# Kernel tuning notes

Measured on AMD Instinct MI355X. Metric: run time of the kernel, lower is better.

## Reference

```python
import jax, jax.numpy as jnp
import numpy as np

TAU = 0.001
TEMPERATURE = 0.1


def setup_inputs() -> dict:
    key = jax.random.key(0)
    k1, k2 = jax.random.split(key)
    B, H, N, L = 2, 8, 256, 64
    X = jax.random.normal(k1, (B, H, N, L), dtype=jnp.float32)
    Y = jax.random.normal(k2, (B, H, N, L), dtype=jnp.float32)
    return {"X": X, "Y": Y}


def _softsort_p2(scores):
    # scores: [B,H,N,L] -> s: [B,H,L,N]
    s = jnp.transpose(scores, (0, 1, 3, 2))
    srt = -jnp.sort(-s, axis=-1)  # descending sort along N
    # pairwise squared diff: rows = sorted values, cols = original values -> [B,H,L,N,N]
    pd = -((s[..., None, :] - srt[..., :, None]) ** 2) / TAU
    return jax.nn.softmax(pd, axis=-1)


def reference(X, Y):
    # Soft permutation matrices: [B,H,L,N,N]
    Pu = _softsort_p2(X)
    Pv = _softsort_p2(Y)
    # Gamma = Pu^T @ Pv  (contract over sorted-row index i)
    Gamma = jnp.einsum('bhlij,bhlik->bhljk', Pu, Pv)
    # cdist(X, Y, p=2) over last dim L -> [B,H,N,N]
    x2 = jnp.sum(X * X, axis=-1)            # [B,H,N]
    y2 = jnp.sum(Y * Y, axis=-1)            # [B,H,N]
    xy = jnp.einsum('bhnl,bhml->bhnm', X, Y)
    cost = jnp.sqrt(jnp.maximum(x2[..., :, None] + y2[..., None, :] - 2.0 * xy, 1e-12))
    # swds[b,h,l] = sum_{j,k} cost[b,h,j,k] * Gamma[b,h,l,j,k]
    swds = jnp.einsum('bhjk,bhljk->bhl', cost, Gamma)
    # exp(-T*(swds - min)) / sum == softmax(-T * swds) over L
    weights = jax.nn.softmax(-TEMPERATURE * swds, axis=-1)  # [B,H,L]
    # weighted sum over L -> [B,H,N,N]
    return jnp.einsum('bhljk,bhl->bhjk', Gamma, weights)
```

## Files before the change

### kernel.cpp

```cpp
#include <hip/hip_runtime.h>
#include <math.h>

#define INV_TAU 1000.0f
#define TEMP    0.1f
#define CEXP    -1442.6950408889634f
#define SQRTC   37.98283767f


typedef __attribute__((ext_vector_type(8))) _Float16 half8;
typedef __attribute__((ext_vector_type(8))) short short8;
typedef __attribute__((ext_vector_type(4))) float f32x4;
typedef __attribute__((ext_vector_type(2))) unsigned int u32x2;

__device__ __forceinline__ float fexp2(float x) { return __builtin_amdgcn_exp2f(x); }

__device__ __forceinline__ half8 ldsh8(const unsigned short* p) {
  return __builtin_bit_cast(half8, *(const short8*)p);
}

__device__ __forceinline__ unsigned bf16r(float f) {
  unsigned u = __float_as_uint(f);
  return (u + 0x7FFFu + ((u >> 16) & 1u)) >> 16;
}

__device__ __forceinline__ int tswz(int row, int g) {
  return row * 32 + (((g + (row >> 1)) & 3) << 3);
}

__global__ __launch_bounds__(256) void prep_kernel(const float* __restrict__ X,
                                                   const float* __restrict__ Y,
                                                   float* __restrict__ cost,
                                                   float* __restrict__ nssu, float* __restrict__ lziu,
                                                   float* __restrict__ nssv, float* __restrict__ lziv) {
  __shared__ __align__(16) float smem[256];
  const int tid = threadIdx.x;
  if (blockIdx.x < 1024) {
    const int jq = blockIdx.x & 63, bh = blockIdx.x >> 6;
    const int j0 = jq * 4;
    smem[tid] = X[((size_t)bh*256 + j0 + (tid >> 6))*64 + (tid & 63)];
    __syncthreads();
    const float4* yp = (const float4*)(Y + ((size_t)bh*256 + tid)*64);
    float dot[4] = {0.f,0.f,0.f,0.f}, x2[4] = {0.f,0.f,0.f,0.f}, y2 = 0.f;
#pragma unroll
    for (int t = 0; t < 16; ++t) {
      float4 yv = yp[t];
      y2 += yv.x*yv.x + yv.y*yv.y + yv.z*yv.z + yv.w*yv.w;
#pragma unroll
      for (int r = 0; r < 4; ++r) {
        float4 xv = ((const float4*)(smem + r*64))[t];
        dot[r] += xv.x*yv.x + xv.y*yv.y + xv.z*yv.z + xv.w*yv.w;
        x2[r]  += xv.x*xv.x + xv.y*xv.y + xv.z*xv.z + xv.w*xv.w;
      }
    }
#pragma unroll
    for (int r = 0; r < 4; ++r) {
      float c = x2[r] + y2 - 2.f*dot[r];
      cost[((size_t)bh*256 + j0 + r)*256 + tid] = sqrtf(fmaxf(c, 1e-12f));
    }
  } else {
    const int idx = blockIdx.x - 1024;
    const int l = idx & 63, bh = (idx >> 6) & 15, uv = idx >> 10;
    const float* S = uv ? Y : X;
    float* so = uv ? nssv : nssu;
    float* zo = uv ? lziv : lziu;
    float v = S[((size_t)bh*256 + tid)*64 + l];
#pragma unroll
    for (int k = 2; k <= 256; k <<= 1) {
#pragma unroll
      for (int j = k >> 1; j > 0; j >>= 1) {
        float o;
        if (j >= 64) {
          smem[tid] = v; __syncthreads();
          o = smem[tid ^ j]; __syncthreads();
        } else {
          o = __shfl_xor(v, j, 64);
        }
        const bool up    = ((tid & k) == 0);
        const bool lower = ((tid & j) == 0);
        float mn = fminf(v, o), mx = fmaxf(v, o);
        v = (up == lower) ? mn : mx;
      }
    }
    smem[tid] = v; __syncthreads();
    const int jc = 255 - tid;
    const float sv = smem[jc];
    const int lo = jc > 48 ? jc - 48 : 0;
    const int hi = jc < 207 ? jc + 48 : 255;
    float z = 0.f;
    for (int jj = lo; jj <= hi; ++jj) { float d = smem[jj] - sv; z += fexp2(d*d*CEXP); }
    const int base = (bh*64 + l)*256 + tid;
    so[base] = -SQRTC * sv; zo[base] = -__log2f(z);
  }
}

__device__ __forceinline__ void stage_slab(int t, int ib, float usc, float vsc,
                                           const float* __restrict__ nssU, const float* __restrict__ lzU,
                                           const float* __restrict__ nssV, const float* __restrict__ lzV,
                                           unsigned short* __restrict__ EU,
                                           unsigned short* __restrict__ EV) {
  {
    const int r = t & 127, g = t >> 7;
    const int i0 = ib + (g << 3);
    float e[8];
#pragma unroll
    for (int ii = 0; ii < 8; ++ii) {
      float d = usc + nssU[i0 + ii];
      e[ii] = fexp2(fmaf(-d, d, lzU[i0 + ii]));
    }
    uint4 w;
    w.x = __builtin_bit_cast(unsigned, __builtin_amdgcn_cvt_pkrtz(e[0], e[1]));
    w.y = __builtin_bit_cast(unsigned, __builtin_amdgcn_cvt_pkrtz(e[2], e[3]));
    w.z = __builtin_bit_cast(unsigned, __builtin_amdgcn_cvt_pkrtz(e[4], e[5]));
    w.w = __builtin_bit_cast(unsigned, __builtin_amdgcn_cvt_pkrtz(e[6], e[7]));
    *(uint4*)&EU[tswz(r, g)] = w;
  }
  {
    const int r = t & 255;
    const int gp = (t >> 8) << 1;
#pragma unroll
    for (int gg = 0; gg < 2; ++gg) {
      const int i0 = ib + ((gp + gg) << 3);
      float e[8];
#pragma unroll
      for (int ii = 0; ii < 8; ++ii) {
        float d = vsc + nssV[i0 + ii];
        e[ii] = fexp2(fmaf(-d, d, lzV[i0 + ii]));
      }
      uint4 w;
      w.x = __builtin_bit_cast(unsigned, __builtin_amdgcn_cvt_pkrtz(e[0], e[1]));
      w.y = __builtin_bit_cast(unsigned, __builtin_amdgcn_cvt_pkrtz(e[2], e[3]));
      w.z = __builtin_bit_cast(unsigned, __builtin_amdgcn_cvt_pkrtz(e[4], e[5]));
      w.w = __builtin_bit_cast(unsigned, __builtin_amdgcn_cvt_pkrtz(e[6], e[7]));
      *(uint4*)&EV[tswz(r, gp + gg)] = w;
    }
  }
}

__global__ __launch_bounds__(512, 4) void pass1_kernel(
    const float* __restrict__ X, const float* __restrict__ Y,
    const float* __restrict__ cost,
    const float* __restrict__ nssu, const float* __restrict__ lziu,
    const float* __restrict__ nssv, const float* __restrict__ lziv,
    float* __restrict__ parts, u32x2* __restrict__ gamma) {
  const int sb = blockIdx.x, l = blockIdx.y, bh = blockIdx.z;
  const int j0 = sb * 128;
  const int tid = threadIdx.x, wave = tid >> 6, lane = tid & 63;
  const int wj = (wave & 1) * 64, wk = (wave >> 1) * 64;
  const int m = lane & 15, q = lane >> 4;
  const int inner = m*32 + (((q + (m >> 1)) & 3) << 3);

  __shared__ float nssU[256], lzU[256], nssV[256], lzV[256];
  __shared__ __align__(16) unsigned short EU0[128*32], EU1[128*32];
  __shared__ __align__(16) unsigned short EV0[256*32], EV1[256*32];
  __shared__ float red[8];

  const int lb = (bh*64 + l)*256;
  const float usc = SQRTC * X[((size_t)bh*256 + j0 + (tid & 127))*64 + l];
  const float vsc = SQRTC * Y[((size_t)bh*256 + (tid & 255))*64 + l];
  if (tid < 256) { nssU[tid] = nssu[lb + tid]; lzU[tid] = lziu[lb + tid]; }
  else { const int t2 = tid - 256; nssV[t2] = nssv[lb + t2]; lzV[t2] = lziv[lb + t2]; }

  f32x4 acc[16];
#pragma unroll
  for (int t = 0; t < 16; ++t) acc[t] = (f32x4){0.f, 0.f, 0.f, 0.f};

  __syncthreads();
  stage_slab(tid, 0, usc, vsc, nssU, lzU, nssV, lzV, EU0, EV0);
  __syncthreads();
#pragma unroll 1
  for (int s = 0; s < 8; ++s) {
    const unsigned short* EUc = (s & 1) ? EU1 : EU0;
    const unsigned short* EVc = (s & 1) ? EV1 : EV0;
    unsigned short* EUn = (s & 1) ? EU0 : EU1;
    unsigned short* EVn = (s & 1) ? EV0 : EV1;
    half8 A[4], B[4];
#pragma unroll
    for (int mt = 0; mt < 4; ++mt) A[mt] = ldsh8(&EUc[(wj + mt*16)*32 + inner]);
#pragma unroll
    for (int nt = 0; nt < 4; ++nt) B[nt] = ldsh8(&EVc[(wk + nt*16)*32 + inner]);
    if (s < 7)
      stage_slab(tid, (s+1)*32, usc, vsc, nssU, lzU, nssV, lzV, EUn, EVn);
#pragma unroll
    for (int mt = 0; mt < 4; ++mt)
#pragma unroll
      for (int nt = 0; nt < 4; ++nt)
        acc[mt*4+nt] = __builtin_amdgcn_mfma_f32_16x16x32_f16(A[mt], B[nt], acc[mt*4+nt], 0, 0, 0);
    __syncthreads();
  }

  const float* cb = cost + (size_t)bh * 65536;
  const int gbase = ((bh*2 + sb)*8 + wave) * 16;
  float part = 0.f;
#pragma unroll
  for (int mt = 0; mt < 4; ++mt) {
#pragma unroll
    for (int nt = 0; nt < 4; ++nt) {
      const int col  = wk + nt*16 + m;
      const int rowb = j0 + wj + mt*16 + q*4;
      f32x4 a = acc[mt*4 + nt];
      part += a.x*cb[(size_t)(rowb+0)*256 + col] + a.y*cb[(size_t)(rowb+1)*256 + col]
            + a.z*cb[(size_t)(rowb+2)*256 + col] + a.w*cb[(size_t)(rowb+3)*256 + col];
      u32x2 pk;
      pk.x = bf16r(a.x) | (bf16r(a.y) << 16);
      pk.y = bf16r(a.z) | (bf16r(a.w) << 16);
      __builtin_nontemporal_store(pk, &gamma[((size_t)(gbase + mt*4 + nt)*64 + l)*64 + lane]);
    }
  }
#pragma unroll
  for (int o = 32; o > 0; o >>= 1) part += __shfl_down(part, o, 64);
  if (lane == 0) red[wave] = part;
  __syncthreads();
  if (tid == 0) {
    float s8 = red[0]+red[1]+red[2]+red[3]+red[4]+red[5]+red[6]+red[7];
    parts[sb*1024 + bh*64 + l] = s8;
  }
}

__global__ __launch_bounds__(256) void wsum_kernel(const u32x2* __restrict__ g,
                                                   const float* __restrict__ parts,
                                                   float* __restrict__ out) {
  const int wv = threadIdx.x >> 6, lane = threadIdx.x & 63;
  const int bh = blockIdx.x >> 6;
  __shared__ float w[64];
  if (wv == 0) {
    float s = parts[bh*64 + lane] + parts[1024 + bh*64 + lane];
    float v = -TEMP * s * 1.4426950408889634f;
    float mx = v;
#pragma unroll
    for (int o = 32; o > 0; o >>= 1) mx = fmaxf(mx, __shfl_xor(mx, o, 64));
    float e = fexp2(v - mx);
    float ssum = e;
#pragma unroll
    for (int o = 32; o > 0; o >>= 1) ssum += __shfl_xor(ssum, o, 64);
    w[lane] = e / ssum;
  }
  __syncthreads();
  const int group = blockIdx.x * 4 + wv;
  const u32x2* gp = g + (size_t)group*4096 + lane;
  float4 acc = {0.f, 0.f, 0.f, 0.f};
#pragma unroll 8
  for (int l = 0; l < 64; ++l) {
    u32x2 pk = __builtin_nontemporal_load(gp + l*64);
    float wl = w[l];
    acc.x += wl * __uint_as_float(pk.x << 16);
    acc.y += wl * __uint_as_float(pk.x & 0xFFFF0000u);
    acc.z += wl * __uint_as_float(pk.y << 16);
    acc.w += wl * __uint_as_float(pk.y & 0xFFFF0000u);
  }
  const int frag = group & 15;
  const int idx  = group >> 4;
  const int wave = idx & 7, sbb = (idx >> 3) & 1;
  const int mt = frag >> 2, nt = frag & 3;
  const int m = lane & 15, q = lane >> 4;
  const int row = sbb*128 + (wave & 1)*64 + mt*16 + q*4;
  const int col = (wave >> 1)*64 + nt*16 + m;
  float* ob = out + ((size_t)bh*256 + row)*256 + col;
  __builtin_nontemporal_store(acc.x, &ob[0]);
  __builtin_nontemporal_store(acc.y, &ob[256]);
  __builtin_nontemporal_store(acc.z, &ob[512]);
  __builtin_nontemporal_store(acc.w, &ob[768]);
}

extern "C" void kernel_launch(void* const* d_in, const int* in_sizes, int n_in,
                              void* d_out, int out_size, void* d_ws, size_t ws_size,
                              hipStream_t stream) {
  (void)in_sizes; (void)n_in; (void)out_size; (void)ws_size;
  const float* X = (const float*)d_in[0];
  const float* Y = (const float*)d_in[1];
  float* out = (float*)d_out;
  float* ws  = (float*)d_ws;
  float* cost  = ws;
  float* nssu  = ws   + 1048576;
  float* lziu  = nssu + 262144;
  float* nssv  = lziu + 262144;
  float* lziv  = nssv + 262144;
  float* parts = lziv + 262144;
  u32x2* gamma = (u32x2*)(parts + 2048);

  prep_kernel <<<dim3(3072),      256, 0, stream>>>(X, Y, cost, nssu, lziu, nssv, lziv);
  pass1_kernel<<<dim3(2, 64, 16), 512, 0, stream>>>(X, Y, cost, nssu, lziu, nssv, lziv,
                                                    parts, gamma);
  wsum_kernel <<<dim3(1024),      256, 0, stream>>>(gamma, parts, out);
}
```

Before: 162.8 us.

## Fuse prep, pass1 and weighted-sum into one cooperative persistent kernel

```diff
diff --git a/kernel.cpp b/kernel.cpp
--- a/kernel.cpp
+++ b/kernel.cpp
@@ -1,10 +1,13 @@
 #include <hip/hip_runtime.h>
+#include <hip/hip_cooperative_groups.h>
 #include <math.h>
 
-#define INV_TAU 1000.0f
+namespace cg = cooperative_groups;
+
 #define TEMP    0.1f
 #define CEXP    -1442.6950408889634f
 #define SQRTC   37.98283767f
+#define LOG2E   1.4426950408889634f
 
 
 typedef __attribute__((ext_vector_type(8))) _Float16 half8;
@@ -27,70 +30,78 @@
   return row * 32 + (((g + (row >> 1)) & 3) << 3);
 }
 
-__global__ __launch_bounds__(256) void prep_kernel(const float* __restrict__ X,
-                                                   const float* __restrict__ Y,
-                                                   float* __restrict__ cost,
-                                                   float* __restrict__ nssu, float* __restrict__ lziu,
-                                                   float* __restrict__ nssv, float* __restrict__ lziv) {
-  __shared__ __align__(16) float smem[256];
-  const int tid = threadIdx.x;
-  if (blockIdx.x < 1024) {
-    const int jq = blockIdx.x & 63, bh = blockIdx.x >> 6;
-    const int j0 = jq * 4;
-    smem[tid] = X[((size_t)bh*256 + j0 + (tid >> 6))*64 + (tid & 63)];
-    __syncthreads();
-    const float4* yp = (const float4*)(Y + ((size_t)bh*256 + tid)*64);
-    float dot[4] = {0.f,0.f,0.f,0.f}, x2[4] = {0.f,0.f,0.f,0.f}, y2 = 0.f;
-#pragma unroll
-    for (int t = 0; t < 16; ++t) {
-      float4 yv = yp[t];
-      y2 += yv.x*yv.x + yv.y*yv.y + yv.z*yv.z + yv.w*yv.w;
-#pragma unroll
-      for (int r = 0; r < 4; ++r) {
-        float4 xv = ((const float4*)(smem + r*64))[t];
-        dot[r] += xv.x*yv.x + xv.y*yv.y + xv.z*yv.z + xv.w*yv.w;
-        x2[r]  += xv.x*xv.x + xv.y*xv.y + xv.z*xv.z + xv.w*xv.w;
+#define LDS_BYTES 53280
+
+__device__ __forceinline__ void cost_unit(int u, int tid, float* smemAll,
+                                          const float* __restrict__ X,
+                                          const float* __restrict__ Y,
+                                          float* __restrict__ cost) {
+  const int half = tid >> 8, t = tid & 255;
+  float* smem = smemAll + half*256;
+  const int jq = u & 63, bh = u >> 6;
+  const int j0 = jq * 4;
+  __syncthreads();
+  smem[t] = X[((size_t)bh*256 + j0 + (t >> 6))*64 + (t & 63)];
+  __syncthreads();
+  const float4* yp = (const float4*)(Y + ((size_t)bh*256 + t)*64);
+  float dot[4] = {0.f,0.f,0.f,0.f}, x2[4] = {0.f,0.f,0.f,0.f}, y2 = 0.f;
+#pragma unroll
+  for (int q = 0; q < 16; ++q) {
+    float4 yv = yp[q];
+    y2 += yv.x*yv.x + yv.y*yv.y + yv.z*yv.z + yv.w*yv.w;
+#pragma unroll
+    for (int r = 0; r < 4; ++r) {
+      float4 xv = ((const float4*)(smem + r*64))[q];
+      dot[r] += xv.x*yv.x + xv.y*yv.y + xv.z*yv.z + xv.w*yv.w;
+      x2[r]  += xv.x*xv.x + xv.y*xv.y + xv.z*xv.z + xv.w*xv.w;
+    }
+  }
+#pragma unroll
+  for (int r = 0; r < 4; ++r) {
+    float c = x2[r] + y2 - 2.f*dot[r];
+    cost[((size_t)bh*256 + j0 + r)*256 + t] = sqrtf(fmaxf(c, 1e-12f));
+  }
+}
+
+__device__ __forceinline__ void sortz_unit(int u, int tid, float* smemAll,
+                                           const float* __restrict__ X,
+                                           const float* __restrict__ Y,
+                                           float* __restrict__ nssu, float* __restrict__ lziu,
+                                           float* __restrict__ nssv, float* __restrict__ lziv) {
+  const int half = tid >> 8, t = tid & 255;
+  float* s = smemAll + half*256;
+  const int l = u & 63, bh = (u >> 6) & 15, uv = u >> 10;
+  const float* S = uv ? Y : X;
+  float* so = uv ? nssv : nssu;
+  float* zo = uv ? lziv : lziu;
+  float v = S[((size_t)bh*256 + t)*64 + l];
+  __syncthreads();
+#pragma unroll
+  for (int k = 2; k <= 256; k <<= 1) {
+#pragma unroll
+    for (int j = k >> 1; j > 0; j >>= 1) {
+      float o;
+      if (j >= 64) {
+        s[t] = v; __syncthreads();
+        o = s[t ^ j]; __syncthreads();
+      } else {
+        o = __shfl_xor(v, j, 64);
       }
-    }
-#pragma unroll
-    for (int r = 0; r < 4; ++r) {
-      float c = x2[r] + y2 - 2.f*dot[r];
-      cost[((size_t)bh*256 + j0 + r)*256 + tid] = sqrtf(fmaxf(c, 1e-12f));
-    }
-  } else {
-    const int idx = blockIdx.x - 1024;
-    const int l = idx & 63, bh = (idx >> 6) & 15, uv = idx >> 10;
-    const float* S = uv ? Y : X;
-    float* so = uv ? nssv : nssu;
-    float* zo = uv ? lziv : lziu;
-    float v = S[((size_t)bh*256 + tid)*64 + l];
-#pragma unroll
-    for (int k = 2; k <= 256; k <<= 1) {
-#pragma unroll
-      for (int j = k >> 1; j > 0; j >>= 1) {
-        float o;
-        if (j >= 64) {
-          smem[tid] = v; __syncthreads();
-          o = smem[tid ^ j]; __syncthreads();
-        } else {
-          o = __shfl_xor(v, j, 64);
-        }
-        const bool up    = ((tid & k) == 0);
-        const bool lower = ((tid & j) == 0);
-        float mn = fminf(v, o), mx = fmaxf(v, o);
-        v = (up == lower) ? mn : mx;
-      }
-    }
-    smem[tid] = v; __syncthreads();
-    const int jc = 255 - tid;
-    const float sv = smem[jc];
-    const int lo = jc > 48 ? jc - 48 : 0;
-    const int hi = jc < 207 ? jc + 48 : 255;
-    float z = 0.f;
-    for (int jj = lo; jj <= hi; ++jj) { float d = smem[jj] - sv; z += fexp2(d*d*CEXP); }
-    const int base = (bh*64 + l)*256 + tid;
-    so[base] = -SQRTC * sv; zo[base] = -__log2f(z);
-  }
+      const bool up    = ((t & k) == 0);
+      const bool lower = ((t & j) == 0);
+      float mn = fminf(v, o), mx = fmaxf(v, o);
+      v = (up == lower) ? mn : mx;
+    }
+  }
+  s[t] = v; __syncthreads();
+  const int jc = 255 - t;
+  const float sv = s[jc];
+  const int lo = jc > 48 ? jc - 48 : 0;
+  const int hi = jc < 207 ? jc + 48 : 255;
+  float z = 0.f;
+  for (int jj = lo; jj <= hi; ++jj) { float d = s[jj] - sv; z += fexp2(d*d*CEXP); }
+  const int base = (bh*64 + l)*256 + t;
+  so[base] = -SQRTC * sv; zo[base] = -__log2f(z);
 }
 
 __device__ __forceinline__ void stage_slab(int t, int ib, float usc, float vsc,
@@ -136,27 +147,33 @@
   }
 }
 
-__global__ __launch_bounds__(512, 4) void pass1_kernel(
+__device__ __forceinline__ void pass1_unit(int unit, int tid, unsigned char* lds,
     const float* __restrict__ X, const float* __restrict__ Y,
     const float* __restrict__ cost,
     const float* __restrict__ nssu, const float* __restrict__ lziu,
     const float* __restrict__ nssv, const float* __restrict__ lziv,
     float* __restrict__ parts, u32x2* __restrict__ gamma) {
-  const int sb = blockIdx.x, l = blockIdx.y, bh = blockIdx.z;
+  float* nssU = (float*)lds;
+  float* lzU  = nssU + 256;
+  float* nssV = lzU + 256;
+  float* lzV  = nssV + 256;
+  float* red  = (float*)(lds + 4096);
+  unsigned short* EU0 = (unsigned short*)(lds + 4128);
+  unsigned short* EU1 = (unsigned short*)(lds + 12320);
+  unsigned short* EV0 = (unsigned short*)(lds + 20512);
+  unsigned short* EV1 = (unsigned short*)(lds + 36896);
+
+  const int sb = unit & 1, l = (unit >> 1) & 63, bh = unit >> 7;
   const int j0 = sb * 128;
-  const int tid = threadIdx.x, wave = tid >> 6, lane = tid & 63;
+  const int wave = tid >> 6, lane = tid & 63;
   const int wj = (wave & 1) * 64, wk = (wave >> 1) * 64;
   const int m = lane & 15, q = lane >> 4;
   const int inner = m*32 + (((q + (m >> 1)) & 3) << 3);
 
-  __shared__ float nssU[256], lzU[256], nssV[256], lzV[256];
-  __shared__ __align__(16) unsigned short EU0[128*32], EU1[128*32];
-  __shared__ __align__(16) unsigned short EV0[256*32], EV1[256*32];
-  __shared__ float red[8];
-
   const int lb = (bh*64 + l)*256;
   const float usc = SQRTC * X[((size_t)bh*256 + j0 + (tid & 127))*64 + l];
   const float vsc = SQRTC * Y[((size_t)bh*256 + (tid & 255))*64 + l];
+  __syncthreads();
   if (tid < 256) { nssU[tid] = nssu[lb + tid]; lzU[tid] = lziu[lb + tid]; }
   else { const int t2 = tid - 256; nssV[t2] = nssv[lb + t2]; lzV[t2] = lziv[lb + t2]; }
 
@@ -211,20 +228,19 @@
   if (lane == 0) red[wave] = part;
   __syncthreads();
   if (tid == 0) {
-    float s8 = red[0]+red[1]+red[2]+red[3]+red[4]+red[5]+red[6]+red[7];
-    parts[sb*1024 + bh*64 + l] = s8;
-  }
-}
-
-__global__ __launch_bounds__(256) void wsum_kernel(const u32x2* __restrict__ g,
-                                                   const float* __restrict__ parts,
-                                                   float* __restrict__ out) {
-  const int wv = threadIdx.x >> 6, lane = threadIdx.x & 63;
-  const int bh = blockIdx.x >> 6;
-  __shared__ float w[64];
-  if (wv == 0) {
+    parts[sb*1024 + bh*64 + l] =
+        red[0]+red[1]+red[2]+red[3]+red[4]+red[5]+red[6]+red[7];
+  }
+}
+
+__device__ __forceinline__ void weights_all(int tid, float* w_all,
+                                            const float* __restrict__ parts) {
+  const int wv = tid >> 6, lane = tid & 63;
+#pragma unroll
+  for (int it = 0; it < 2; ++it) {
+    const int bh = wv + it*8;
     float s = parts[bh*64 + lane] + parts[1024 + bh*64 + lane];
-    float v = -TEMP * s * 1.4426950408889634f;
+    float v = -TEMP * s * LOG2E;
     float mx = v;
 #pragma unroll
     for (int o = 32; o > 0; o >>= 1) mx = fmaxf(mx, __shfl_xor(mx, o, 64));
@@ -232,10 +248,17 @@
     float ssum = e;
 #pragma unroll
     for (int o = 32; o > 0; o >>= 1) ssum += __shfl_xor(ssum, o, 64);
-    w[lane] = e / ssum;
-  }
-  __syncthreads();
-  const int group = blockIdx.x * 4 + wv;
+    w_all[bh*64 + lane] = e / ssum;
+  }
+}
+
+__device__ __forceinline__ void wsum_group(int group, int lane, const float* w_all,
+                                           const u32x2* __restrict__ g,
+                                           float* __restrict__ out) {
+  const int frag = group & 15;
+  const int idx  = group >> 4;
+  const int wave = idx & 7, sbb = (idx >> 3) & 1, bh = idx >> 4;
+  const float* w = w_all + bh*64;
   const u32x2* gp = g + (size_t)group*4096 + lane;
   float4 acc = {0.f, 0.f, 0.f, 0.f};
 #pragma unroll 8
@@ -247,9 +270,6 @@
     acc.z += wl * __uint_as_float(pk.y << 16);
     acc.w += wl * __uint_as_float(pk.y & 0xFFFF0000u);
   }
-  const int frag = group & 15;
-  const int idx  = group >> 4;
-  const int wave = idx & 7, sbb = (idx >> 3) & 1;
   const int mt = frag >> 2, nt = frag & 3;
   const int m = lane & 15, q = lane >> 4;
   const int row = sbb*128 + (wave & 1)*64 + mt*16 + q*4;
@@ -259,6 +279,86 @@
   __builtin_nontemporal_store(acc.y, &ob[256]);
   __builtin_nontemporal_store(acc.z, &ob[512]);
   __builtin_nontemporal_store(acc.w, &ob[768]);
+}
+
+__global__ __launch_bounds__(512, 4) void fused_kernel(
+    const float* __restrict__ X, const float* __restrict__ Y,
+    float* __restrict__ cost,
+    float* __restrict__ nssu, float* __restrict__ lziu,
+    float* __restrict__ nssv, float* __restrict__ lziv,
+    float* __restrict__ parts, u32x2* __restrict__ gamma,
+    float* __restrict__ out) {
+  __shared__ __align__(16) unsigned char lds[LDS_BYTES];
+  const int tid = threadIdx.x;
+  float* smemAll = (float*)lds;
+
+  {
+    const int nsub = gridDim.x * 2;
+    const int sub0 = blockIdx.x*2 + (tid >> 8);
+    const int it1 = (1024 + nsub - 1) / nsub;
+    for (int it = 0; it < it1; ++it) {
+      int u = sub0 + it*nsub; if (u > 1023) u = 1023;
+      cost_unit(u, tid, smemAll, X, Y, cost);
+    }
+    const int it2 = (2048 + nsub - 1) / nsub;
+    for (int it = 0; it < it2; ++it) {
+      int u = sub0 + it*nsub; if (u > 2047) u = 2047;
+      sortz_unit(u, tid, smemAll, X, Y, nssu, lziu, nssv, lziv);
+    }
+  }
+  cg::this_grid().sync();
+
+  {
+    const int iters = (2048 + gridDim.x - 1) / gridDim.x;
+    for (int it = 0; it < iters; ++it) {
+      int u = blockIdx.x + it*gridDim.x; if (u > 2047) u = 2047;
+      pass1_unit(u, tid, lds, X, Y, cost, nssu, lziu, nssv, lziv, parts, gamma);
+    }
+  }
+  cg::this_grid().sync();
+
+  {
+    float* w_all = (float*)lds;
+    weights_all(tid, w_all, parts);
+    __syncthreads();
+    const int wv = tid >> 6, lane = tid & 63;
+    const int nwu = gridDim.x * 8;
+    const int iters = (4096 + nwu - 1) / nwu;
+    for (int it = 0; it < iters; ++it) {
+      int gidx = blockIdx.x*8 + wv + it*nwu; if (gidx > 4095) gidx = 4095;
+      wsum_group(gidx, lane, w_all, gamma, out);
+    }
+  }
+}
+
+__global__ __launch_bounds__(512) void k_prep(const float* __restrict__ X,
+                                              const float* __restrict__ Y,
+                                              float* __restrict__ cost,
+                                              float* __restrict__ nssu, float* __restrict__ lziu,
+                                              float* __restrict__ nssv, float* __restrict__ lziv) {
+  __shared__ __align__(16) float smemAll[512];
+  const int sub = blockIdx.x*2 + (threadIdx.x >> 8);
+  if (sub < 1024) cost_unit(sub, threadIdx.x, smemAll, X, Y, cost);
+  else            sortz_unit(sub - 1024, threadIdx.x, smemAll, X, Y, nssu, lziu, nssv, lziv);
+}
+
+__global__ __launch_bounds__(512, 4) void k_pass1(
+    const float* __restrict__ X, const float* __restrict__ Y,
+    const float* __restrict__ cost,
+    const float* __restrict__ nssu, const float* __restrict__ lziu,
+    const float* __restrict__ nssv, const float* __restrict__ lziv,
+    float* __restrict__ parts, u32x2* __restrict__ gamma) {
+  __shared__ __align__(16) unsigned char lds[LDS_BYTES];
+  pass1_unit(blockIdx.x, threadIdx.x, lds, X, Y, cost, nssu, lziu, nssv, lziv, parts, gamma);
+}
+
+__global__ __launch_bounds__(512) void k_wsum(const u32x2* __restrict__ g,
+                                              const float* __restrict__ parts,
+                                              float* __restrict__ out) {
+  __shared__ float w_all[1024];
+  weights_all(threadIdx.x, w_all, parts);
+  __syncthreads();
+  wsum_group(blockIdx.x*8 + (threadIdx.x >> 6), threadIdx.x & 63, w_all, g, out);
 }
 
 extern "C" void kernel_launch(void* const* d_in, const int* in_sizes, int n_in,
@@ -277,8 +377,29 @@
   float* parts = lziv + 262144;
   u32x2* gamma = (u32x2*)(parts + 2048);
 
-  prep_kernel <<<dim3(3072),      256, 0, stream>>>(X, Y, cost, nssu, lziu, nssv, lziv);
-  pass1_kernel<<<dim3(2, 64, 16), 512, 0, stream>>>(X, Y, cost, nssu, lziu, nssv, lziv,
-                                                    parts, gamma);
-  wsum_kernel <<<dim3(1024),      256, 0, stream>>>(gamma, parts, out);
-}
+  static int coop_grid = -1;
+  if (coop_grid < 0) {
+    int occ = 0;
+    hipError_t e = hipOccupancyMaxActiveBlocksPerMultiprocessor(&occ, fused_kernel, 512, 0);
+    int g = (e == hipSuccess) ? occ * 256 : 0;
+    if (g > 512) g = 512;
+    coop_grid = g;
+  }
+
+  bool done = false;
+  if (coop_grid > 0) {
+    void* args[] = { (void*)&X, (void*)&Y, (void*)&cost,
+                     (void*)&nssu, (void*)&lziu, (void*)&nssv, (void*)&lziv,
+                     (void*)&parts, (void*)&gamma, (void*)&out };
+    hipError_t e = hipLaunchCooperativeKernel((const void*)fused_kernel,
+                                              dim3(coop_grid), dim3(512),
+                                              args, 0, stream);
+    done = (e == hipSuccess);
+  }
+  if (!done) {
+    k_prep <<<dim3(1536),       512, 0, stream>>>(X, Y, cost, nssu, lziu, nssv, lziv);
+    k_pass1<<<dim3(2048),       512, 0, stream>>>(X, Y, cost, nssu, lziu, nssv, lziv,
+                                                  parts, gamma);
+    k_wsum <<<dim3(512),        512, 0, stream>>>(gamma, parts, out);
+  }
+}
```

Result: slower. 347.0 us (+113.1%).
